# Kernel optimization log

Hardware: AMD Instinct MI355X
Metric: run time of the kernel (lower is better)

## Reference

```python
import jax, jax.numpy as jnp
import numpy as np

T, B, V, H, L = 512, 64, 256, 1024, 3


def setup_inputs() -> dict:
    key = jax.random.key(0)
    ks = jax.random.split(key, 12)
    s = 1.0 / np.sqrt(H)
    # one-hot character inputs, padded to (T, B, V)
    tokens = jax.random.randint(ks[0], (T, B), 0, V)
    inputs = jax.nn.one_hot(tokens, V, dtype=jnp.float32)
    # descending lengths, max length == T (as produced by sort + pad_sequence)
    lengths = jnp.sort(jax.random.randint(ks[1], (B,), T // 2, T + 1))[::-1]
    lengths = lengths.at[0].set(T)
    u = lambda k, shape: jax.random.uniform(k, shape, jnp.float32, -s, s)
    return {
        "inputs": inputs,
        "lengths": lengths,
        "Wih0": u(ks[2], (4 * H, V)),
        "Whh0": u(ks[3], (4 * H, H)),
        "bih0": u(ks[4], (4 * H,)),
        "bhh0": u(ks[5], (4 * H,)),
        "Wih_rest": u(ks[6], (L - 1, 4 * H, H)),
        "Whh_rest": u(ks[7], (L - 1, 4 * H, H)),
        "bih_rest": u(ks[8], (L - 1, 4 * H)),
        "bhh_rest": u(ks[9], (L - 1, 4 * H)),
        "Wout": u(ks[10], (V, H)),
        "bout": u(ks[11], (V,)),
    }


def _lstm_cell(x, h, c, Wih, Whh, bih, bhh):
    # PyTorch LSTMCell gate order: i, f, g, o
    gates = x @ Wih.T + h @ Whh.T + bih + bhh
    i, f, g, o = jnp.split(gates, 4, axis=-1)
    c2 = jax.nn.sigmoid(f) * c + jax.nn.sigmoid(i) * jnp.tanh(g)
    h2 = jax.nn.sigmoid(o) * jnp.tanh(c2)
    return h2, c2


def reference(inputs, lengths, Wih0, Whh0, bih0, bhh0,
              Wih_rest, Whh_rest, bih_rest, bhh_rest, Wout, bout):
    Tn, Bn, _ = inputs.shape
    L_rest = Wih_rest.shape[0]
    Hn = Whh0.shape[1]
    h0 = jnp.zeros((1 + L_rest, Bn, Hn), inputs.dtype)
    c0 = jnp.zeros_like(h0)
    # mask[t, b] = 1 while sequence b is active; equivalent to i_active slicing
    mask = (jnp.arange(Tn)[:, None] < lengths[None, :]).astype(inputs.dtype)

    def step(carry, xt_mt):
        h, c = carry
        xt, mt = xt_mt
        hs, cs = [], []
        hn, cn = _lstm_cell(xt, h[0], c[0], Wih0, Whh0, bih0, bhh0)
        hs.append(hn); cs.append(cn)
        inp = hn
        for l in range(L_rest):  # fixed small layer count
            hn, cn = _lstm_cell(inp, h[l + 1], c[l + 1],
                                Wih_rest[l], Whh_rest[l], bih_rest[l], bhh_rest[l])
            hs.append(hn); cs.append(cn)
            inp = hn
        out = inp * mt[:, None]  # padded timesteps -> zeros (pad_sequence)
        return (jnp.stack(hs), jnp.stack(cs)), out

    _, ys = jax.lax.scan(step, (h0, c0), (inputs, mask))  # ys: [T, B, H]
    logits = ys @ Wout.T + bout  # [T, B, V]
    return jnp.transpose(logits, (1, 2, 0))  # (batch, vocab, time)
```

## Files before the change

kernel.cpp:

```cpp
#include <hip/hip_runtime.h>
#include <stdint.h>

#define T_ 512
#define B_ 64
#define V_ 256
#define H_ 1024
#define KMAX 2048

typedef short short8 __attribute__((ext_vector_type(8)));
typedef float float4_ __attribute__((ext_vector_type(4)));
typedef unsigned short ushort_t;
typedef unsigned long long ull;

__device__ __forceinline__ float sigf(float x){ return 1.0f/(1.0f + __expf(-x)); }
__device__ __forceinline__ float tanhfast(float x){ return 1.0f - 2.0f/(__expf(2.0f*x) + 1.0f); }
__device__ __forceinline__ ushort_t f2bf(float x){
  uint32_t u = __float_as_uint(x);
  uint32_t r = (u + 0x7FFFu + ((u >> 16) & 1u)) >> 16;
  return (ushort_t)r;
}

__global__ void k_cvt(const float* __restrict__ in, ushort_t* __restrict__ out, int n){
  int i = blockIdx.x*256 + threadIdx.x;
  if (i < n) out[i] = f2bf(in[i]);
}

__global__ void k_pack0(const float* __restrict__ Wih0, const float* __restrict__ Whh0,
                        ushort_t* __restrict__ Wpk){
  int i = blockIdx.x*256 + threadIdx.x;
  if (i >= 4096*2048) return;
  int p = i >> 11, k = i & 2047;
  int col = (p & 3)*1024 + (p >> 2);
  float v = (k < 256) ? Wih0[col*256 + k] : (k < 1024 ? 0.0f : Whh0[col*1024 + (k - 1024)]);
  Wpk[i] = f2bf(v);
}

__global__ void k_pack12(const float* __restrict__ Wih, const float* __restrict__ Whh,
                         ushort_t* __restrict__ Wpk){
  int i = blockIdx.x*256 + threadIdx.x;
  if (i >= 4096*2048) return;
  int p = i >> 11, k = i & 2047;
  int col = (p & 3)*1024 + (p >> 2);
  float v = (k < 1024) ? Wih[col*1024 + k] : Whh[col*1024 + (k - 1024)];
  Wpk[i] = f2bf(v);
}

__global__ void k_bias(const float* __restrict__ bih0, const float* __restrict__ bhh0,
                       const float* __restrict__ bihR, const float* __restrict__ bhhR,
                       float* __restrict__ biaspk){
  int i = blockIdx.x*256 + threadIdx.x;
  if (i >= 3*4096) return;
  int l = i >> 12, p = i & 4095;
  int col = (p & 3)*1024 + (p >> 2);
  float v = (l == 0) ? (bih0[col] + bhh0[col])
                     : (bihR[(l-1)*4096 + col] + bhhR[(l-1)*4096 + col]);
  biaspk[i] = v;
}

__global__ void k_zero(ull* __restrict__ h, int n_ull, int* __restrict__ flags, int nf){
  int i = blockIdx.x*256 + threadIdx.x;
  if (i < n_ull) h[i] = 0ull;
  if (i < nf) flags[i] = 0;
}

__global__ __launch_bounds__(256, 1) void k_lstm(
    const ushort_t* __restrict__ xin,
    const ushort_t* __restrict__ Wpk0,
    const ushort_t* __restrict__ Wpk1,
    const ushort_t* __restrict__ Wpk2,
    const float*  __restrict__ biaspk,
    ushort_t* ypp,
    ushort_t* y2,
    ull* hbuf,
    int* flags)
{
  const int tid  = threadIdx.x;
  const int lane = tid & 63;
  const int wv   = tid >> 6;
  const int g    = blockIdx.x >> 6;
  const int cb   = blockIdx.x & 63;
  const int p0   = cb * 64;
  const int j0   = cb * 16;

  const int kxend = (g == 0) ? 256 : 1024;
  const int sx    = (g == 0) ? 256 : 1024;
  const ushort_t* xbase = (g == 0) ? xin : ypp + (size_t)(g - 1) * 2 * B_ * H_;
  ushort_t* ybase       = (g == 2) ? y2  : ypp + (size_t)g * 2 * B_ * H_;
  const ushort_t* Wpk  = (g == 0) ? Wpk0 : (g == 1 ? Wpk1 : Wpk2);
  const float* bias = biaspk + g*4096;
  ull* hb0 = hbuf + (size_t)g * 2 * (B_*H_/4);

  const int ks = wv * 512;

  short8 breg[8][4][2];
  #pragma unroll
  for (int c = 0; c < 8; ++c){
    #pragma unroll
    for (int ct = 0; ct < 4; ++ct){
      const ushort_t* pb = Wpk + (size_t)(p0 + ct*16 + (lane & 15)) * KMAX
                               + (ks + c*64) + ((lane >> 4) << 3);
      breg[c][ct][0] = *(const short8*)pb;
      breg[c][ct][1] = *(const short8*)(pb + 32);
    }
  }

  __shared__ float red[2][64][68];

  const int eb = tid >> 2;
  const int jq = tid & 3;
  float c_reg[4] = {0.f, 0.f, 0.f, 0.f};

  for (int s = 0; s < T_ + 2; ++s){
    int t = s - g;
    if (t >= 0 && t < T_){
      const ushort_t* xt = (g == 0) ? xbase + (size_t)t * B_ * 256
                                    : xbase + (size_t)(t & 1) * B_ * H_;
      ushort_t* yt       = (g == 2) ? ybase + (size_t)t * B_ * H_
                                    : ybase + (size_t)(t & 1) * B_ * H_;
      const ushort_t* hcur = (const ushort_t*)(hb0 + (size_t)(t & 1) * (B_*H_/4));
      ull* hnxt = hb0 + (size_t)((t + 1) & 1) * (B_*H_/4);

      float4_ acc[4][4];
      #pragma unroll
      for (int a = 0; a < 4; ++a)
        #pragma unroll
        for (int b = 0; b < 4; ++b){ float4_ z = {0.f,0.f,0.f,0.f}; acc[a][b] = z; }

      #pragma unroll
      for (int c = 0; c < 8; ++c){
        int k0 = ks + c*64;
        short8 av[4][2];
        bool alive = true;
        if (k0 < 1024){
          if (k0 < kxend){
            #pragma unroll
            for (int bt = 0; bt < 4; ++bt){
              int m = bt*16 + (lane & 15);
              const ushort_t* pa = xt + (size_t)m * sx + k0 + ((lane >> 4) << 3);
              av[bt][0] = *(const short8*)pa;
              av[bt][1] = *(const short8*)(pa + 32);
            }
          } else {
            alive = false;
          }
        } else {
          #pragma unroll
          for (int bt = 0; bt < 4; ++bt){
            int m = bt*16 + (lane & 15);
            const ushort_t* pa = hcur + (size_t)m * 1024 + (k0 - 1024) + ((lane >> 4) << 3);
            av[bt][0] = *(const short8*)pa;
            av[bt][1] = *(const short8*)(pa + 32);
          }
        }
        if (alive){
          #pragma unroll
          for (int ct = 0; ct < 4; ++ct){
            #pragma unroll
            for (int bt = 0; bt < 4; ++bt){
              acc[bt][ct] = __builtin_amdgcn_mfma_f32_16x16x32_bf16(av[bt][0], breg[c][ct][0], acc[bt][ct], 0, 0, 0);
              acc[bt][ct] = __builtin_amdgcn_mfma_f32_16x16x32_bf16(av[bt][1], breg[c][ct][1], acc[bt][ct], 0, 0, 0);
            }
          }
        }
      }

      if (wv < 2){
        #pragma unroll
        for (int bt = 0; bt < 4; ++bt){
          int row = bt*16 + ((lane >> 4) << 2);
          #pragma unroll
          for (int ct = 0; ct < 4; ++ct){
            int colb = ct*16 + (lane & 15);
            #pragma unroll
            for (int r = 0; r < 4; ++r) red[wv][row + r][colb] = acc[bt][ct][r];
          }
        }
      }
      __syncthreads();
      if (wv >= 2){
        #pragma unroll
        for (int bt = 0; bt < 4; ++bt){
          int row = bt*16 + ((lane >> 4) << 2);
          #pragma unroll
          for (int ct = 0; ct < 4; ++ct){
            int colb = ct*16 + (lane & 15);
            #pragma unroll
            for (int r = 0; r < 4; ++r) red[wv - 2][row + r][colb] += acc[bt][ct][r];
          }
        }
      }
      __syncthreads();

      ull hpack = 0ull;
      #pragma unroll
      for (int r = 0; r < 4; ++r){
        int jl = jq*4 + r;
        float4_ a0 = *(float4_*)&red[0][eb][jl*4];
        float4_ a1 = *(float4_*)&red[1][eb][jl*4];
        float4_ bsv = *(const float4_*)(bias + p0 + jl*4);
        float4_ gsv = a0 + a1 + bsv;
        float iv = sigf(gsv.x);
        float fv = sigf(gsv.y);
        float gv = tanhfast(gsv.z);
        float ov = sigf(gsv.w);
        float cv = fv * c_reg[r] + iv * gv;
        c_reg[r] = cv;
        float hv = ov * tanhfast(cv);
        hpack |= ((ull)f2bf(hv)) << (16 * r);
      }
      size_t eo = (size_t)eb * 1024 + j0 + jq*4;
      __hip_atomic_store(hnxt + (eo >> 2), hpack, __ATOMIC_RELAXED, __HIP_MEMORY_SCOPE_AGENT);
      if (g == 2){
        *(ull*)(yt + eo) = hpack;
      } else {
        __hip_atomic_store((ull*)(yt + eo), hpack, __ATOMIC_RELAXED, __HIP_MEMORY_SCOPE_AGENT);
      }
    }

    __syncthreads();
    if (tid == 0){
      __hip_atomic_store(flags + (size_t)blockIdx.x * 16, s + 1,
                         __ATOMIC_RELAXED, __HIP_MEMORY_SCOPE_AGENT);
    }
    asm volatile("" ::: "memory");
    if (tid < 192){
      const int* fp = flags + (size_t)tid * 16;
      while (__hip_atomic_load(fp, __ATOMIC_RELAXED, __HIP_MEMORY_SCOPE_AGENT) < s + 1){
        __builtin_amdgcn_s_sleep(8);
      }
    }
    __syncthreads();
    __builtin_amdgcn_fence(__ATOMIC_ACQUIRE, "agent");
  }
}

__global__ __launch_bounds__(256, 1) void k_out(
    const ushort_t* __restrict__ y2, const ushort_t* __restrict__ Woutb,
    const float* __restrict__ bout, const int* __restrict__ lengths,
    float* __restrict__ dout)
{
  int tid = threadIdx.x, lane = tid & 63, wv = tid >> 6;
  int bid = blockIdx.x;
  int b = bid >> 5;
  int rem = bid & 31;
  int vv = rem >> 3, tt = rem & 7;
  int t0 = tt*64 + wv*16;
  float4_ acc[4];
  #pragma unroll
  for (int i = 0; i < 4; ++i){ float4_ z = {0.f,0.f,0.f,0.f}; acc[i] = z; }
  int m = lane & 15, kq = lane >> 4;
  const ushort_t* ya = y2 + ((size_t)(t0 + m) * B_ + b) * H_ + (kq << 3);
  for (int k0 = 0; k0 < 1024; k0 += 32){
    short8 af = *(const short8*)(ya + k0);
    #pragma unroll
    for (int ct = 0; ct < 4; ++ct){
      int v = vv*64 + ct*16 + m;
      short8 bf = *(const short8*)(Woutb + (size_t)v * H_ + k0 + (kq << 3));
      acc[ct] = __builtin_amdgcn_mfma_f32_16x16x32_bf16(af, bf, acc[ct], 0, 0, 0);
    }
  }
  int len = lengths[b];
  int tb = t0 + (kq << 2);
  #pragma unroll
  for (int ct = 0; ct < 4; ++ct){
    int v = vv*64 + ct*16 + m;
    float bo = bout[v];
    float4_ res;
    #pragma unroll
    for (int r = 0; r < 4; ++r){
      int tcur = tb + r;
      res[r] = (tcur < len) ? (acc[ct][r] + bo) : bo;
    }
    *(float4_*)(dout + ((size_t)b * V_ + v) * T_ + tb) = res;
  }
}

extern "C" void kernel_launch(void* const* d_in, const int* in_sizes, int n_in,
                              void* d_out, int out_size, void* d_ws, size_t ws_size,
                              hipStream_t stream){
  const float* inputs = (const float*)d_in[0];
  const int*   lengths= (const int*)d_in[1];
  const float* Wih0 = (const float*)d_in[2];
  const float* Whh0 = (const float*)d_in[3];
  const float* bih0 = (const float*)d_in[4];
  const float* bhh0 = (const float*)d_in[5];
  const float* WihR = (const float*)d_in[6];
  const float* WhhR = (const float*)d_in[7];
  const float* bihR = (const float*)d_in[8];
  const float* bhhR = (const float*)d_in[9];
  const float* Wout = (const float*)d_in[10];
  const float* bout = (const float*)d_in[11];
  float* out = (float*)d_out;

  char* ws = (char*)d_ws;
  size_t off = 0;
  auto alloc = [&](size_t bytes) -> void* {
    void* p = ws + off; off += (bytes + 255) & ~(size_t)255; return p;
  };
  ushort_t* xin   = (ushort_t*)alloc((size_t)T_*B_*V_*2);
  ushort_t* ypp   = (ushort_t*)alloc((size_t)2*2*B_*H_*2);
  ushort_t* y2    = (ushort_t*)alloc((size_t)T_*B_*H_*2);
  ushort_t* Wpk0  = (ushort_t*)alloc((size_t)4096*2048*2);
  ushort_t* Wpk1  = (ushort_t*)alloc((size_t)4096*2048*2);
  ushort_t* Wpk2  = (ushort_t*)alloc((size_t)4096*2048*2);
  ushort_t* Woutb = (ushort_t*)alloc((size_t)256*1024*2);
  float*    biaspk= (float*)alloc((size_t)3*4096*4);
  ull*      hbuf  = (ull*)alloc((size_t)3*2*(B_*H_/4)*8);
  int*      flags = (int*)alloc(16384);

  int n;
  n = T_*B_*V_;   k_cvt<<<(n+255)/256, 256, 0, stream>>>(inputs, xin, n);
  n = 256*1024;   k_cvt<<<(n+255)/256, 256, 0, stream>>>(Wout, Woutb, n);
  n = 4096*2048;  k_pack0<<<(n+255)/256, 256, 0, stream>>>(Wih0, Whh0, Wpk0);
  k_pack12<<<(n+255)/256, 256, 0, stream>>>(WihR, WhhR, Wpk1);
  k_pack12<<<(n+255)/256, 256, 0, stream>>>(WihR + (size_t)4096*1024,
                                            WhhR + (size_t)4096*1024, Wpk2);
  n = 3*4096;     k_bias<<<(n+255)/256, 256, 0, stream>>>(bih0, bhh0, bihR, bhhR, biaspk);
  { int nz = 3*2*(B_*H_/4); k_zero<<<(nz+255)/256, 256, 0, stream>>>(hbuf, nz, flags, 4096); }

  k_lstm<<<192, 256, 0, stream>>>(xin, Wpk0, Wpk1, Wpk2, biaspk, ypp, y2, hbuf, flags);
  k_out<<<2048, 256, 0, stream>>>(y2, Woutb, bout, lengths, out);
}
```

Baseline: 8.531 ms.

## Double-buffer activation loads and narrow the cross-block wait to dependent groups

The activation-fragment loads in the recurrent LSTM kernel are now software-pipelined: the loads for chunk c+1 are issued before the MFMAs for chunk c, so load latency can overlap with compute. The per-step grid barrier now only waits on the flags of the layer groups each block actually depends on, not all 192 blocks. The spin sleep is also shortened from 8 to 1. Together these aim to cut per-timestep latency on the serial critical path. The costs are more register pressure from the doubled A buffers and more polling traffic. The narrower wait also relies on the ping-pong buffers being safe without global lockstep.

```diff
diff --git a/kernel.cpp b/kernel.cpp
--- a/kernel.cpp
+++ b/kernel.cpp
@@ -62,6 +62,27 @@
   if (i < n_ull) h[i] = 0ull;
   if (i < nf) flags[i] = 0;
 }
+
+#define LOAD_CHUNK(cc, buf)                                                   \
+  { int k0_ = ks + (cc)*64;                                                   \
+    if (k0_ < kxend){                                                         \
+      _Pragma("unroll")                                                       \
+      for (int bt_ = 0; bt_ < 4; ++bt_){                                      \
+        int m_ = bt_*16 + (lane & 15);                                        \
+        const ushort_t* pa_ = xt + (size_t)m_ * sx + k0_ + ((lane >> 4) << 3);\
+        buf[bt_][0] = *(const short8*)pa_;                                    \
+        buf[bt_][1] = *(const short8*)(pa_ + 32);                             \
+      }                                                                       \
+    } else if (k0_ >= 1024){                                                  \
+      _Pragma("unroll")                                                       \
+      for (int bt_ = 0; bt_ < 4; ++bt_){                                      \
+        int m_ = bt_*16 + (lane & 15);                                        \
+        const ushort_t* pa_ = hcur + (size_t)m_ * 1024 + (k0_ - 1024)         \
+                                   + ((lane >> 4) << 3);                      \
+        buf[bt_][0] = *(const short8*)pa_;                                    \
+        buf[bt_][1] = *(const short8*)(pa_ + 32);                             \
+      }                                                                       \
+    } }
 
 __global__ __launch_bounds__(256, 1) void k_lstm(
     const ushort_t* __restrict__ xin,
@@ -110,6 +131,8 @@
   const int jq = tid & 3;
   float c_reg[4] = {0.f, 0.f, 0.f, 0.f};
 
+  const bool care = (tid < 192) && ((g == 0) ? (tid < 128) : (g == 1 ? true : (tid >= 64)));
+
   for (int s = 0; s < T_ + 2; ++s){
     int t = s - g;
     if (t >= 0 && t < T_){
@@ -126,39 +149,19 @@
         #pragma unroll
         for (int b = 0; b < 4; ++b){ float4_ z = {0.f,0.f,0.f,0.f}; acc[a][b] = z; }
 
+      short8 av[2][4][2];
+      LOAD_CHUNK(0, av[0]);
       #pragma unroll
       for (int c = 0; c < 8; ++c){
+        if (c < 7){ LOAD_CHUNK(c + 1, av[(c + 1) & 1]); }
         int k0 = ks + c*64;
-        short8 av[4][2];
-        bool alive = true;
-        if (k0 < 1024){
-          if (k0 < kxend){
-            #pragma unroll
-            for (int bt = 0; bt < 4; ++bt){
-              int m = bt*16 + (lane & 15);
-              const ushort_t* pa = xt + (size_t)m * sx + k0 + ((lane >> 4) << 3);
-              av[bt][0] = *(const short8*)pa;
-              av[bt][1] = *(const short8*)(pa + 32);
-            }
-          } else {
-            alive = false;
-          }
-        } else {
-          #pragma unroll
-          for (int bt = 0; bt < 4; ++bt){
-            int m = bt*16 + (lane & 15);
-            const ushort_t* pa = hcur + (size_t)m * 1024 + (k0 - 1024) + ((lane >> 4) << 3);
-            av[bt][0] = *(const short8*)pa;
-            av[bt][1] = *(const short8*)(pa + 32);
-          }
-        }
-        if (alive){
+        if (k0 < kxend || k0 >= 1024){
           #pragma unroll
           for (int ct = 0; ct < 4; ++ct){
             #pragma unroll
             for (int bt = 0; bt < 4; ++bt){
-              acc[bt][ct] = __builtin_amdgcn_mfma_f32_16x16x32_bf16(av[bt][0], breg[c][ct][0], acc[bt][ct], 0, 0, 0);
-              acc[bt][ct] = __builtin_amdgcn_mfma_f32_16x16x32_bf16(av[bt][1], breg[c][ct][1], acc[bt][ct], 0, 0, 0);
+              acc[bt][ct] = __builtin_amdgcn_mfma_f32_16x16x32_bf16(av[c & 1][bt][0], breg[c][ct][0], acc[bt][ct], 0, 0, 0);
+              acc[bt][ct] = __builtin_amdgcn_mfma_f32_16x16x32_bf16(av[c & 1][bt][1], breg[c][ct][1], acc[bt][ct], 0, 0, 0);
             }
           }
         }
@@ -223,10 +226,10 @@
                          __ATOMIC_RELAXED, __HIP_MEMORY_SCOPE_AGENT);
     }
     asm volatile("" ::: "memory");
-    if (tid < 192){
+    if (care){
       const int* fp = flags + (size_t)tid * 16;
       while (__hip_atomic_load(fp, __ATOMIC_RELAXED, __HIP_MEMORY_SCOPE_AGENT) < s + 1){
-        __builtin_amdgcn_s_sleep(8);
+        __builtin_amdgcn_s_sleep(1);
       }
     }
     __syncthreads();
```

After: 8.600 ms. Within noise of the previous version (+0.8%).
